# Optimization experiments

Hardware: AMD Instinct MI355X
Metric: run time of the kernel (lower is better)

Reference implementation:

```python
import jax, jax.numpy as jnp
import numpy as np

D_MODEL = 1024
N_HEADS = 16
D_K = D_MODEL // N_HEADS
THETA = 10000.0
MAX_SEQ = 2048


def _trunc_normal(key, shape, std):
    # approximate trunc_normal in [-3std, 3std] via clipping (init only; values irrelevant to math)
    return jnp.clip(jax.random.normal(key, shape) * std, -3 * std, 3 * std).astype(jnp.float32)


def setup_inputs() -> dict:
    key = jax.random.key(0)
    kx, kq, kk, kv, ko = jax.random.split(key, 5)
    std = np.sqrt(2.0 / (D_MODEL + D_MODEL))
    x = jax.random.normal(kx, (2, 2048, D_MODEL), dtype=jnp.float32)
    W_q = _trunc_normal(kq, (D_MODEL, D_MODEL), std)
    W_k = _trunc_normal(kk, (D_MODEL, D_MODEL), std)
    W_v = _trunc_normal(kv, (D_MODEL, D_MODEL), std)
    W_o = _trunc_normal(ko, (D_MODEL, D_MODEL), std)
    return {"x": x, "W_q": W_q, "W_k": W_k, "W_v": W_v, "W_o": W_o}


def _rope(x, positions):
    # x: [b, n, s, d_k]; interleaved even/odd pairing: (x0,x1),(x2,x3),...
    d = x.shape[-1]
    inv_freq = THETA ** (-2.0 * jnp.arange(0, d // 2, dtype=jnp.float32) / d)
    angles = positions.astype(jnp.float32)[:, None] * inv_freq[None, :]  # [s, d/2]
    cos, sin = jnp.cos(angles), jnp.sin(angles)
    xp = x.reshape(x.shape[:-1] + (d // 2, 2))
    x_even, x_odd = xp[..., 0], xp[..., 1]
    out_even = x_even * cos - x_odd * sin
    out_odd = x_even * sin + x_odd * cos
    return jnp.stack((out_even, out_odd), axis=-1).reshape(x.shape)


def reference(x, W_q, W_k, W_v, W_o):
    b, s, _ = x.shape
    def split_heads(t):
        return t.reshape(b, s, N_HEADS, D_K).transpose(0, 2, 1, 3)  # b n s d
    Q = split_heads(x @ W_q.T)
    K = split_heads(x @ W_k.T)
    V = split_heads(x @ W_v.T)
    pos = jnp.arange(s)
    Q = _rope(Q, pos)
    K = _rope(K, pos)
    score = jnp.einsum('bnqd,bnkd->bnqk', Q, K) / jnp.sqrt(jnp.float32(D_K))
    causal = jnp.triu(jnp.ones((s, s), dtype=bool), k=1)
    score = jnp.where(causal[None, None], -jnp.inf, score)
    attn = jax.nn.softmax(score, axis=-1)
    out = jnp.einsum('bnqk,bnkd->bnqd', attn, V)
    out = out.transpose(0, 2, 1, 3).reshape(b, s, D_MODEL)
    return out @ W_o.T
```

## Files before the change

### kernel.cpp

```cpp
#include <hip/hip_runtime.h>

typedef float f32x4 __attribute__((ext_vector_type(4)));
typedef __bf16 bf16x8 __attribute__((ext_vector_type(8)));

#define D_MODEL 1024
#define SEQ     2048
#define NB      2
#define NH      16
#define DK      64

__device__ __forceinline__ unsigned short f2bf(float f) {
    union { float f; unsigned int u; } un; un.f = f;
    unsigned int r = un.u + 0x7fffu + ((un.u >> 16) & 1u);
    return (unsigned short)(r >> 16);
}

__device__ __forceinline__ unsigned cvtpk(float lo, float hi) {
    unsigned r;
    asm("v_cvt_pk_bf16_f32 %0, %1, %2" : "=v"(r) : "v"(lo), "v"(hi));
    return r;
}

__device__ __forceinline__ void gload16(const void* g, void* l) {
    __builtin_amdgcn_global_load_lds((__attribute__((address_space(1))) void*)g,
                                     (__attribute__((address_space(3))) void*)l,
                                     16, 0, 0);
}

__global__ __launch_bounds__(256) void cast5(
    const float* __restrict__ x,  const float* __restrict__ wq,
    const float* __restrict__ wk, const float* __restrict__ wv,
    const float* __restrict__ wo,
    unsigned short* __restrict__ xb,  unsigned short* __restrict__ wqb,
    unsigned short* __restrict__ wkb, unsigned short* __restrict__ wvb,
    unsigned short* __restrict__ wob, float2* __restrict__ tab)
{
    if (blockIdx.y == 5) {
        int idx = blockIdx.x * 256 + threadIdx.x;
        if (idx < SEQ * 32) {
            int ss = idx >> 5, p = idx & 31;
            float freq = exp2f(-0.41524101186f * (float)p);
            float sn, cs;
            sincosf((float)ss * freq, &sn, &cs);
            tab[idx] = make_float2(cs, sn);
        }
        return;
    }
    const float* src; unsigned short* dst; int n8;
    switch (blockIdx.y) {
        case 0:  src = x;  dst = xb;  n8 = (NB*SEQ*D_MODEL)/8; break;
        case 1:  src = wq; dst = wqb; n8 = (D_MODEL*D_MODEL)/8; break;
        case 2:  src = wk; dst = wkb; n8 = (D_MODEL*D_MODEL)/8; break;
        case 3:  src = wv; dst = wvb; n8 = (D_MODEL*D_MODEL)/8; break;
        default: src = wo; dst = wob; n8 = (D_MODEL*D_MODEL)/8; break;
    }
    int stride = gridDim.x * blockDim.x;
    for (int i = blockIdx.x * blockDim.x + threadIdx.x; i < n8; i += stride) {
        const float4* p = (const float4*)src + (size_t)i * 2;
        float4 a = p[0], b = p[1];
        union { unsigned short h[8]; uint4 v; } u;
        u.h[0] = f2bf(a.x); u.h[1] = f2bf(a.y); u.h[2] = f2bf(a.z); u.h[3] = f2bf(a.w);
        u.h[4] = f2bf(b.x); u.h[5] = f2bf(b.y); u.h[6] = f2bf(b.z); u.h[7] = f2bf(b.w);
        ((uint4*)dst)[i] = u.v;
    }
}

template <int MODE, int BM, int BN>
__global__ __launch_bounds__(256) void gemm_bt(
    const unsigned short* __restrict__ A,
    const unsigned short* __restrict__ B0,
    const unsigned short* __restrict__ B1,
    const unsigned short* __restrict__ B2,
    float* __restrict__ outF,
    unsigned short* __restrict__ Qh,
    unsigned short* __restrict__ Kh,
    unsigned short* __restrict__ Vt,
    const float2* __restrict__ tab,
    int M, int K)
{
    constexpr int PER_STAGE = (BM + BN) / 64;
    constexpr int WM = BM / 2, WN = BN / 2;
    constexpr int FM = WM / 16, FN = WN / 16;
    __shared__ __align__(16) unsigned short SM[3 * (BM + BN) * 32];

    const int lane = threadIdx.x & 63;
    const int wid  = threadIdx.x >> 6;
    const int l15 = lane & 15, lhi = lane >> 4;

    const int L  = blockIdx.x;
    const int yl = L & 7;
    const int t  = L >> 3;
    const int bx = t & 7;
    const int t2 = t >> 3;
    int y, z;
    if constexpr (MODE == 1) { y = ((t2 & 3) << 3) | yl; z = t2 >> 2; }
    else                     { y = (t2 << 3) | yl;       z = 0;       }
    const int m0 = y * BM;
    const int n0 = bx * BN;
    const unsigned short* B = (z == 0) ? B0 : (z == 1) ? B1 : B2;
    const int waveM = (wid >> 1) * WM;
    const int waveN = (wid & 1) * WN;

    f32x4 acc[FM][FN];
    f32x4 zero = {0.f, 0.f, 0.f, 0.f};
#pragma unroll
    for (int m = 0; m < FM; ++m)
#pragma unroll
        for (int n = 0; n < FN; ++n) acc[m][n] = zero;

    const int lrow = lane >> 2;
    const int lcol = (lane & 3) * 8;

    auto STAGE = [&](int buf, int k0) {
        unsigned short* as = SM + buf * (BM + BN) * 32;
        unsigned short* bs = as + BM * 32;
#pragma unroll
        for (int q = 0; q < BM / 64; ++q) {
            int rbase = wid * (BM / 4) + q * 16;
            gload16(A + (size_t)(m0 + rbase + lrow) * K + k0 + lcol,
                    (char*)as + rbase * 64);
        }
#pragma unroll
        for (int q = 0; q < BN / 64; ++q) {
            int rbase = wid * (BN / 4) + q * 16;
            gload16(B + (size_t)(n0 + rbase + lrow) * K + k0 + lcol,
                    (char*)bs + rbase * 64);
        }
    };

    const int NK = K >> 5;
    STAGE(0, 0);
    STAGE(1, 32);

    for (int k = 0; k < NK; ++k) {
        if (k < NK - 1) {
            if constexpr (PER_STAGE == 4) asm volatile("s_waitcnt vmcnt(4)" ::: "memory");
            else                          asm volatile("s_waitcnt vmcnt(3)" ::: "memory");
        } else {
            asm volatile("s_waitcnt vmcnt(0)" ::: "memory");
        }
        __builtin_amdgcn_s_barrier();
        __builtin_amdgcn_sched_barrier(0);
        if (k + 2 < NK) STAGE((k + 2) % 3, (k + 2) << 5);

        const unsigned short* as = SM + (k % 3) * (BM + BN) * 32;
        const unsigned short* bs = as + BM * 32;
        bf16x8 af[FM], bfr[FN];
#pragma unroll
        for (int m = 0; m < FM; ++m)
            af[m] = *(const bf16x8*)(as + (waveM + m * 16 + l15) * 32 + lhi * 8);
#pragma unroll
        for (int n = 0; n < FN; ++n)
            bfr[n] = *(const bf16x8*)(bs + (waveN + n * 16 + l15) * 32 + lhi * 8);
        __builtin_amdgcn_s_setprio(1);
#pragma unroll
        for (int m = 0; m < FM; ++m)
#pragma unroll
            for (int n = 0; n < FN; ++n)
                acc[m][n] = __builtin_amdgcn_mfma_f32_16x16x32_bf16(af[m], bfr[n], acc[m][n], 0, 0, 0);
        __builtin_amdgcn_s_setprio(0);
    }

    if constexpr (MODE == 0) {
#pragma unroll
        for (int n = 0; n < FN; ++n) {
            int col = n0 + waveN + n * 16 + l15;
#pragma unroll
            for (int m = 0; m < FM; ++m) {
                int rowb = m0 + waveM + m * 16 + (lhi << 2);
#pragma unroll
                for (int r = 0; r < 4; ++r)
                    outF[(size_t)(rowb + r) * D_MODEL + col] = acc[m][n][r];
            }
        }
    } else {
        __syncthreads();
        unsigned short* Ct = ((unsigned short*)SM) + wid * 4608;
        const int colg0 = n0 + waveN;
        const int hh    = (colg0 >> 6) & (NH - 1);
        const int rowg0 = m0 + waveM;
        const int bb    = rowg0 >> 11;
        const size_t bhh = (size_t)(bb * NH + hh);

#pragma unroll
        for (int n = 0; n < 4; ++n) {
            int cl = n * 16 + l15;
#pragma unroll
            for (int m = 0; m < 4; ++m) {
#pragma unroll
                for (int r = 0; r < 4; ++r) {
                    float v  = acc[m][n][r];
                    float pv = __shfl_xor(v, 1);
                    int rl = m * 16 + (lhi << 2) + r;
                    if (z == 2) {
                        Ct[cl * 72 + rl] = f2bf(v);
                    } else {
                        int ss = (rowg0 + rl) & (SEQ - 1);
                        float2 cs = tab[(ss << 5) + (cl >> 1)];
                        float o = (cl & 1) ? (pv * cs.y + v * cs.x)
                                           : (v * cs.x - pv * cs.y);
                        if (z == 0) o *= 0.18033688011f;
                        Ct[rl * 72 + cl] = f2bf(o);
                    }
                }
            }
        }
        asm volatile("s_waitcnt lgkmcnt(0)" ::: "memory");

        const int lr = lane >> 3;
        const int lc = (lane & 7) << 3;
#pragma unroll
        for (int i = 0; i < 8; ++i) {
            int rl = i * 8 + lr;
            uint4 w = *(const uint4*)&Ct[rl * 72 + lc];
            if (z == 2) {
                int ss0 = rowg0 & (SEQ - 1);
                *(uint4*)(Vt + (bhh * DK + rl) * SEQ + ss0 + lc) = w;
            } else {
                int ss = (rowg0 + rl) & (SEQ - 1);
                unsigned short* dst = (z == 0) ? Qh : Kh;
                *(uint4*)(dst + (bhh * SEQ + ss) * DK + lc) = w;
            }
        }
    }
}

__global__ __launch_bounds__(256) void attn_kernel(
    const unsigned short* __restrict__ Qh,
    const unsigned short* __restrict__ Kh,
    const unsigned short* __restrict__ Vt,
    unsigned short* __restrict__ O)
{
    __shared__ unsigned short Ks[2][64 * 64];
    __shared__ unsigned short Vs[2][64 * 64];
    __shared__ unsigned short P[4][16 * 64];

    const int tid  = threadIdx.x;
    const int lane = tid & 63;
    const int wid  = tid >> 6;
    const int l15 = lane & 15, lhi = lane >> 4;

    const int Bk  = blockIdx.x;
    const int xcd = Bk & 7;
    const int r0  = Bk >> 3;
    const int bh  = (xcd << 2) | (r0 & 3);
    const int yq  = r0 >> 2;
    const int g   = yq >> 3, j = yq & 7;
    const int qt  = (g << 3) + ((g & 1) ? (7 - j) : j);
    const int b = bh >> 4, h = bh & 15;

    const unsigned short* Qb = Qh + (size_t)bh * SEQ * DK;
    const unsigned short* Kb = Kh + (size_t)bh * SEQ * DK;
    const unsigned short* Vb = Vt + (size_t)bh * DK * SEQ;

    auto STAGE = [&](int buf, int kv0s) {
#pragma unroll
        for (int c = 0; c < 2; ++c) {
            int ub = c * 256 + wid * 64;
            int u  = ub + lane;
            int kr = u >> 3;
            int kc = (u & 7) ^ (kr & 7);
            gload16(Kb + (size_t)(kv0s + kr) * DK + kc * 8, &Ks[buf][(size_t)ub * 8]);
        }
#pragma unroll
        for (int c = 0; c < 2; ++c) {
            int ub = c * 256 + wid * 64;
            int u  = ub + lane;
            int vr = u >> 3;
            int vc = (u & 7) ^ (vr & 7);
            gload16(Vb + (size_t)vr * SEQ + kv0s + vc * 8, &Vs[buf][(size_t)ub * 8]);
        }
    };

    const f32x4 zero = {0.f, 0.f, 0.f, 0.f};
    const f32x4 ninf = {-1e30f, -1e30f, -1e30f, -1e30f};

    STAGE(0, 0);
    int cur = 0;

    const int q0 = qt * 64;
    const int qw = q0 + wid * 16;

    bf16x8 qf[2];
#pragma unroll
    for (int kk = 0; kk < 2; ++kk)
        qf[kk] = *(const bf16x8*)(Qb + (size_t)(qw + l15) * DK + kk * 32 + lhi * 8);

    f32x4 oacc[4];
#pragma unroll
    for (int nd = 0; nd < 4; ++nd) oacc[nd] = zero;
    float mrow = -1e30f;
    float lrow = 0.f;

    for (int kt = 0; kt <= qt; ++kt) {
        const int kv0 = kt << 6;
        const bool diag = (kt == qt);
        const int nlim = diag ? (wid + 1) : 4;

        asm volatile("s_waitcnt vmcnt(0)" ::: "memory");
        __builtin_amdgcn_s_barrier();
        __builtin_amdgcn_sched_barrier(0);

        if (kt < qt) STAGE(cur ^ 1, kv0 + 64);

        f32x4 s[4];
#pragma unroll
        for (int n = 0; n < 4; ++n) s[n] = (n < nlim) ? zero : ninf;

        const int sw = l15 & 7;
        __builtin_amdgcn_s_setprio(1);
#pragma unroll
        for (int n = 0; n < 4; ++n) {
            if (n < nlim) {
                int rr = n * 16 + l15;
                bf16x8 k0 = *(const bf16x8*)&Ks[cur][rr * 64 + ((lhi ^ sw) << 3)];
                bf16x8 k1 = *(const bf16x8*)&Ks[cur][rr * 64 + (((4 + lhi) ^ sw) << 3)];
                s[n] = __builtin_amdgcn_mfma_f32_16x16x32_bf16(k0, qf[0], s[n], 0, 0, 0);
                s[n] = __builtin_amdgcn_mfma_f32_16x16x32_bf16(k1, qf[1], s[n], 0, 0, 0);
            }
        }
        __builtin_amdgcn_s_setprio(0);

        if (diag) {
            const int qg = qw + l15;
#pragma unroll
            for (int n = 0; n < 4; ++n) {
                if (n < nlim) {
#pragma unroll
                    for (int rr = 0; rr < 4; ++rr) {
                        int kg = kv0 + n * 16 + (lhi << 2) + rr;
                        if (kg > qg) s[n][rr] = -1e30f;
                    }
                }
            }
        }

        float mx = fmaxf(fmaxf(s[0][0], s[0][1]), fmaxf(s[0][2], s[0][3]));
#pragma unroll
        for (int n = 1; n < 4; ++n)
            mx = fmaxf(mx, fmaxf(fmaxf(s[n][0], s[n][1]), fmaxf(s[n][2], s[n][3])));
        mx = fmaxf(mx, __shfl_xor(mx, 16));
        mx = fmaxf(mx, __shfl_xor(mx, 32));

        float alpha = 1.f;
        const int allDefer = __all(mx <= mrow + 8.f);
        if (!allDefer) {
            float mn = fmaxf(mrow, mx);
            alpha = __builtin_amdgcn_exp2f(mrow - mn);
            mrow = mn;
        }

#pragma unroll
        for (int n = 0; n < 4; ++n)
#pragma unroll
            for (int rr = 0; rr < 4; ++rr)
                s[n][rr] = __builtin_amdgcn_exp2f(s[n][rr] - mrow);

        float rs = 0.f;
#pragma unroll
        for (int n = 0; n < 4; ++n)
            rs += (s[n][0] + s[n][1]) + (s[n][2] + s[n][3]);
        rs += __shfl_xor(rs, 16);
        rs += __shfl_xor(rs, 32);
        lrow = allDefer ? (lrow + rs) : (lrow * alpha + rs);

#pragma unroll
        for (int n = 0; n < 4; ++n) {
            uint2 pk;
            pk.x = cvtpk(s[n][0], s[n][1]);
            pk.y = cvtpk(s[n][2], s[n][3]);
            int cW = 2 * n + (lhi >> 1);
            *(uint2*)&P[wid][(l15 << 6) + ((cW ^ sw) << 3) + ((lhi & 1) << 2)] = pk;
        }

        if (!allDefer) {
            float a0 = __shfl(alpha, (lhi << 2) + 0);
            float a1 = __shfl(alpha, (lhi << 2) + 1);
            float a2 = __shfl(alpha, (lhi << 2) + 2);
            float a3 = __shfl(alpha, (lhi << 2) + 3);
#pragma unroll
            for (int nd = 0; nd < 4; ++nd) {
                oacc[nd][0] *= a0; oacc[nd][1] *= a1;
                oacc[nd][2] *= a2; oacc[nd][3] *= a3;
            }
        }

        asm volatile("s_waitcnt lgkmcnt(0)" ::: "memory");
        const int kklim = diag ? ((nlim + 1) >> 1) : 2;
        bf16x8 pa[2];
#pragma unroll
        for (int kk = 0; kk < 2; ++kk)
            if (kk < kklim)
                pa[kk] = *(const bf16x8*)&P[wid][(l15 << 6) + ((((kk << 2) + lhi) ^ sw) << 3)];

        __builtin_amdgcn_s_setprio(1);
#pragma unroll
        for (int nd = 0; nd < 4; ++nd)
#pragma unroll
            for (int kk = 0; kk < 2; ++kk)
                if (kk < kklim) {
                    int rd = nd * 16 + l15;
                    bf16x8 vf = *(const bf16x8*)&Vs[cur][rd * 64 + ((((kk << 2) + lhi) ^ sw) << 3)];
                    oacc[nd] = __builtin_amdgcn_mfma_f32_16x16x32_bf16(pa[kk], vf, oacc[nd], 0, 0, 0);
                }
        __builtin_amdgcn_s_setprio(0);

        cur ^= 1;
    }

    float inv = 1.f / lrow;
    float i0 = __shfl(inv, (lhi << 2) + 0);
    float i1 = __shfl(inv, (lhi << 2) + 1);
    float i2 = __shfl(inv, (lhi << 2) + 2);
    float i3 = __shfl(inv, (lhi << 2) + 3);
#pragma unroll
    for (int nd = 0; nd < 4; ++nd) {
        int d = nd * 16 + l15;
        int rowb = qw + (lhi << 2);
        O[((size_t)(b * SEQ + rowb + 0)) * D_MODEL + h * DK + d] = f2bf(oacc[nd][0] * i0);
        O[((size_t)(b * SEQ + rowb + 1)) * D_MODEL + h * DK + d] = f2bf(oacc[nd][1] * i1);
        O[((size_t)(b * SEQ + rowb + 2)) * D_MODEL + h * DK + d] = f2bf(oacc[nd][2] * i2);
        O[((size_t)(b * SEQ + rowb + 3)) * D_MODEL + h * DK + d] = f2bf(oacc[nd][3] * i3);
    }
}

extern "C" void kernel_launch(void* const* d_in, const int* in_sizes, int n_in,
                              void* d_out, int out_size, void* d_ws, size_t ws_size,
                              hipStream_t stream)
{
    const float* x  = (const float*)d_in[0];
    const float* Wq = (const float*)d_in[1];
    const float* Wk = (const float*)d_in[2];
    const float* Wv = (const float*)d_in[3];
    const float* Wo = (const float*)d_in[4];
    float* out = (float*)d_out;

    char* ws = (char*)d_ws;
    unsigned short* xb  = (unsigned short*)(ws);
    unsigned short* Wqb = (unsigned short*)(ws + ( 8ull << 20));
    unsigned short* Wkb = (unsigned short*)(ws + (10ull << 20));
    unsigned short* Wvb = (unsigned short*)(ws + (12ull << 20));
    unsigned short* Wob = (unsigned short*)(ws + (14ull << 20));
    unsigned short* Qh  = (unsigned short*)(ws + (16ull << 20));
    unsigned short* Kh  = (unsigned short*)(ws + (24ull << 20));
    unsigned short* Vt  = (unsigned short*)(ws + (32ull << 20));
    float2*         tab = (float2*)(ws + (40ull << 20));
    unsigned short* attn = xb;

    cast5<<<dim3(512, 6), 256, 0, stream>>>(x, Wq, Wk, Wv, Wo, xb, Wqb, Wkb, Wvb, Wob, tab);

    gemm_bt<1, 128, 128><<<768, 256, 0, stream>>>(
        xb, Wqb, Wkb, Wvb, nullptr, Qh, Kh, Vt, tab, NB * SEQ, D_MODEL);

    attn_kernel<<<1024, 256, 0, stream>>>(Qh, Kh, Vt, attn);

    gemm_bt<0, 64, 128><<<512, 256, 0, stream>>>(
        attn, Wob, Wob, Wob, out, nullptr, nullptr, nullptr, nullptr, NB * SEQ, D_MODEL);
}
```

Before: 116.7 us.

## Pair causal q-tiles per block and triple-buffer K/V tiles

Each attention block now handles two query tiles, pi and 31-pi, so every block does the same 33 KV-tile iterations. This balances the causal triangle's work and halves the grid to 512 blocks. The K/V staging moves from double to triple buffering with a lookahead of two tiles and a partial vmcnt wait, which hides more load latency. The cost is more shared memory per block (lower possible occupancy) and fewer blocks to fill the GPU.

Result: no change. 115.9 us (-0.7%).

```diff
diff --git a/kernel.cpp b/kernel.cpp
--- a/kernel.cpp
+++ b/kernel.cpp
@@ -231,8 +231,8 @@
     const unsigned short* __restrict__ Vt,
     unsigned short* __restrict__ O)
 {
-    __shared__ unsigned short Ks[2][64 * 64];
-    __shared__ unsigned short Vs[2][64 * 64];
+    __shared__ unsigned short Ks[3][64 * 64];
+    __shared__ unsigned short Vs[3][64 * 64];
     __shared__ unsigned short P[4][16 * 64];
 
     const int tid  = threadIdx.x;
@@ -240,18 +240,21 @@
     const int wid  = tid >> 6;
     const int l15 = lane & 15, lhi = lane >> 4;
 
-    const int Bk  = blockIdx.x;
-    const int xcd = Bk & 7;
-    const int r0  = Bk >> 3;
+    const int L   = blockIdx.x;
+    const int xcd = L & 7;
+    const int r0  = L >> 3;
     const int bh  = (xcd << 2) | (r0 & 3);
-    const int yq  = r0 >> 2;
-    const int g   = yq >> 3, j = yq & 7;
-    const int qt  = (g << 3) + ((g & 1) ? (7 - j) : j);
+    const int pi  = r0 >> 2;
     const int b = bh >> 4, h = bh & 15;
 
     const unsigned short* Qb = Qh + (size_t)bh * SEQ * DK;
     const unsigned short* Kb = Kh + (size_t)bh * SEQ * DK;
     const unsigned short* Vb = Vt + (size_t)bh * DK * SEQ;
+
+    const int NT0 = pi + 1;
+    const int NTT = 33;
+
+    auto kv_of = [&](int g) { return (g < NT0 ? g : g - NT0) << 6; };
 
     auto STAGE = [&](int buf, int kv0s) {
 #pragma unroll
@@ -261,166 +264,165 @@
             int kr = u >> 3;
             int kc = (u & 7) ^ (kr & 7);
             gload16(Kb + (size_t)(kv0s + kr) * DK + kc * 8, &Ks[buf][(size_t)ub * 8]);
-        }
-#pragma unroll
-        for (int c = 0; c < 2; ++c) {
-            int ub = c * 256 + wid * 64;
-            int u  = ub + lane;
-            int vr = u >> 3;
-            int vc = (u & 7) ^ (vr & 7);
-            gload16(Vb + (size_t)vr * SEQ + kv0s + vc * 8, &Vs[buf][(size_t)ub * 8]);
+            gload16(Vb + (size_t)kr * SEQ + kv0s + kc * 8, &Vs[buf][(size_t)ub * 8]);
         }
     };
 
     const f32x4 zero = {0.f, 0.f, 0.f, 0.f};
     const f32x4 ninf = {-1e30f, -1e30f, -1e30f, -1e30f};
+    const int sw = l15 & 7;
 
     STAGE(0, 0);
-    int cur = 0;
-
-    const int q0 = qt * 64;
-    const int qw = q0 + wid * 16;
-
-    bf16x8 qf[2];
-#pragma unroll
-    for (int kk = 0; kk < 2; ++kk)
-        qf[kk] = *(const bf16x8*)(Qb + (size_t)(qw + l15) * DK + kk * 32 + lhi * 8);
-
-    f32x4 oacc[4];
-#pragma unroll
-    for (int nd = 0; nd < 4; ++nd) oacc[nd] = zero;
-    float mrow = -1e30f;
-    float lrow = 0.f;
-
-    for (int kt = 0; kt <= qt; ++kt) {
-        const int kv0 = kt << 6;
-        const bool diag = (kt == qt);
-        const int nlim = diag ? (wid + 1) : 4;
-
-        asm volatile("s_waitcnt vmcnt(0)" ::: "memory");
-        __builtin_amdgcn_s_barrier();
-        __builtin_amdgcn_sched_barrier(0);
-
-        if (kt < qt) STAGE(cur ^ 1, kv0 + 64);
-
-        f32x4 s[4];
-#pragma unroll
-        for (int n = 0; n < 4; ++n) s[n] = (n < nlim) ? zero : ninf;
-
-        const int sw = l15 & 7;
-        __builtin_amdgcn_s_setprio(1);
-#pragma unroll
-        for (int n = 0; n < 4; ++n) {
-            if (n < nlim) {
-                int rr = n * 16 + l15;
-                bf16x8 k0 = *(const bf16x8*)&Ks[cur][rr * 64 + ((lhi ^ sw) << 3)];
-                bf16x8 k1 = *(const bf16x8*)&Ks[cur][rr * 64 + (((4 + lhi) ^ sw) << 3)];
-                s[n] = __builtin_amdgcn_mfma_f32_16x16x32_bf16(k0, qf[0], s[n], 0, 0, 0);
-                s[n] = __builtin_amdgcn_mfma_f32_16x16x32_bf16(k1, qf[1], s[n], 0, 0, 0);
-            }
-        }
-        __builtin_amdgcn_s_setprio(0);
-
-        if (diag) {
-            const int qg = qw + l15;
+    STAGE(1, kv_of(1));
+    int g = 0;
+
+    for (int ph = 0; ph < 2; ++ph) {
+        const int qt = ph ? (31 - pi) : pi;
+        const int q0 = qt << 6;
+        const int qw = q0 + wid * 16;
+        const int lastkt = qt;
+
+        bf16x8 qf[2];
+#pragma unroll
+        for (int kk = 0; kk < 2; ++kk)
+            qf[kk] = *(const bf16x8*)(Qb + (size_t)(qw + l15) * DK + kk * 32 + lhi * 8);
+
+        f32x4 oacc[4];
+#pragma unroll
+        for (int nd = 0; nd < 4; ++nd) oacc[nd] = zero;
+        float mrow = -1e30f;
+        float lrow = 0.f;
+
+        for (int kt = 0; kt <= lastkt; ++kt, ++g) {
+            const int kv0 = kt << 6;
+            const bool diag = (kt == lastkt);
+            const int nlim = diag ? (wid + 1) : 4;
+
+            if (g < NTT - 1) asm volatile("s_waitcnt vmcnt(4)" ::: "memory");
+            else             asm volatile("s_waitcnt vmcnt(0)" ::: "memory");
+            __builtin_amdgcn_s_barrier();
+            __builtin_amdgcn_sched_barrier(0);
+            if (g + 2 < NTT) STAGE((g + 2) % 3, kv_of(g + 2));
+
+            const unsigned short* Kc = Ks[g % 3];
+            const unsigned short* Vc = Vs[g % 3];
+
+            f32x4 s[4];
+#pragma unroll
+            for (int n = 0; n < 4; ++n) s[n] = (n < nlim) ? zero : ninf;
+
+            __builtin_amdgcn_s_setprio(1);
 #pragma unroll
             for (int n = 0; n < 4; ++n) {
                 if (n < nlim) {
-#pragma unroll
-                    for (int rr = 0; rr < 4; ++rr) {
-                        int kg = kv0 + n * 16 + (lhi << 2) + rr;
-                        if (kg > qg) s[n][rr] = -1e30f;
+                    int rr = n * 16 + l15;
+                    bf16x8 k0 = *(const bf16x8*)&Kc[rr * 64 + ((lhi ^ sw) << 3)];
+                    bf16x8 k1 = *(const bf16x8*)&Kc[rr * 64 + (((4 + lhi) ^ sw) << 3)];
+                    s[n] = __builtin_amdgcn_mfma_f32_16x16x32_bf16(k0, qf[0], s[n], 0, 0, 0);
+                    s[n] = __builtin_amdgcn_mfma_f32_16x16x32_bf16(k1, qf[1], s[n], 0, 0, 0);
+                }
+            }
+            __builtin_amdgcn_s_setprio(0);
+
+            if (diag) {
+                const int qg = qw + l15;
+#pragma unroll
+                for (int n = 0; n < 4; ++n) {
+                    if (n < nlim) {
+#pragma unroll
+                        for (int rr = 0; rr < 4; ++rr) {
+                            int kg = kv0 + n * 16 + (lhi << 2) + rr;
+                            if (kg > qg) s[n][rr] = -1e30f;
+                        }
                     }
                 }
             }
-        }
-
-        float mx = fmaxf(fmaxf(s[0][0], s[0][1]), fmaxf(s[0][2], s[0][3]));
-#pragma unroll
-        for (int n = 1; n < 4; ++n)
-            mx = fmaxf(mx, fmaxf(fmaxf(s[n][0], s[n][1]), fmaxf(s[n][2], s[n][3])));
-        mx = fmaxf(mx, __shfl_xor(mx, 16));
-        mx = fmaxf(mx, __shfl_xor(mx, 32));
-
-        float alpha = 1.f;
-        const int allDefer = __all(mx <= mrow + 8.f);
-        if (!allDefer) {
-            float mn = fmaxf(mrow, mx);
-            alpha = __builtin_amdgcn_exp2f(mrow - mn);
-            mrow = mn;
-        }
-
-#pragma unroll
-        for (int n = 0; n < 4; ++n)
-#pragma unroll
-            for (int rr = 0; rr < 4; ++rr)
-                s[n][rr] = __builtin_amdgcn_exp2f(s[n][rr] - mrow);
-
-        float rs = 0.f;
-#pragma unroll
-        for (int n = 0; n < 4; ++n)
-            rs += (s[n][0] + s[n][1]) + (s[n][2] + s[n][3]);
-        rs += __shfl_xor(rs, 16);
-        rs += __shfl_xor(rs, 32);
-        lrow = allDefer ? (lrow + rs) : (lrow * alpha + rs);
-
-#pragma unroll
-        for (int n = 0; n < 4; ++n) {
-            uint2 pk;
-            pk.x = cvtpk(s[n][0], s[n][1]);
-            pk.y = cvtpk(s[n][2], s[n][3]);
-            int cW = 2 * n + (lhi >> 1);
-            *(uint2*)&P[wid][(l15 << 6) + ((cW ^ sw) << 3) + ((lhi & 1) << 2)] = pk;
-        }
-
-        if (!allDefer) {
-            float a0 = __shfl(alpha, (lhi << 2) + 0);
-            float a1 = __shfl(alpha, (lhi << 2) + 1);
-            float a2 = __shfl(alpha, (lhi << 2) + 2);
-            float a3 = __shfl(alpha, (lhi << 2) + 3);
-#pragma unroll
-            for (int nd = 0; nd < 4; ++nd) {
-                oacc[nd][0] *= a0; oacc[nd][1] *= a1;
-                oacc[nd][2] *= a2; oacc[nd][3] *= a3;
-            }
-        }
-
-        asm volatile("s_waitcnt lgkmcnt(0)" ::: "memory");
-        const int kklim = diag ? ((nlim + 1) >> 1) : 2;
-        bf16x8 pa[2];
-#pragma unroll
-        for (int kk = 0; kk < 2; ++kk)
-            if (kk < kklim)
-                pa[kk] = *(const bf16x8*)&P[wid][(l15 << 6) + ((((kk << 2) + lhi) ^ sw) << 3)];
-
-        __builtin_amdgcn_s_setprio(1);
-#pragma unroll
-        for (int nd = 0; nd < 4; ++nd)
+
+            float mx = fmaxf(fmaxf(s[0][0], s[0][1]), fmaxf(s[0][2], s[0][3]));
+#pragma unroll
+            for (int n = 1; n < 4; ++n)
+                mx = fmaxf(mx, fmaxf(fmaxf(s[n][0], s[n][1]), fmaxf(s[n][2], s[n][3])));
+            mx = fmaxf(mx, __shfl_xor(mx, 16));
+            mx = fmaxf(mx, __shfl_xor(mx, 32));
+
+            float alpha = 1.f;
+            const int allDefer = __all(mx <= mrow + 8.f);
+            if (!allDefer) {
+                float mn = fmaxf(mrow, mx);
+                alpha = __builtin_amdgcn_exp2f(mrow - mn);
+                mrow = mn;
+            }
+
+#pragma unroll
+            for (int n = 0; n < 4; ++n)
+#pragma unroll
+                for (int rr = 0; rr < 4; ++rr)
+                    s[n][rr] = __builtin_amdgcn_exp2f(s[n][rr] - mrow);
+
+            float rs = 0.f;
+#pragma unroll
+            for (int n = 0; n < 4; ++n)
+                rs += (s[n][0] + s[n][1]) + (s[n][2] + s[n][3]);
+            rs += __shfl_xor(rs, 16);
+            rs += __shfl_xor(rs, 32);
+            lrow = allDefer ? (lrow + rs) : (lrow * alpha + rs);
+
+#pragma unroll
+            for (int n = 0; n < 4; ++n) {
+                uint2 pk;
+                pk.x = cvtpk(s[n][0], s[n][1]);
+                pk.y = cvtpk(s[n][2], s[n][3]);
+                int cW = 2 * n + (lhi >> 1);
+                *(uint2*)&P[wid][(l15 << 6) + ((cW ^ sw) << 3) + ((lhi & 1) << 2)] = pk;
+            }
+
+            if (!allDefer) {
+                float a0 = __shfl(alpha, (lhi << 2) + 0);
+                float a1 = __shfl(alpha, (lhi << 2) + 1);
+                float a2 = __shfl(alpha, (lhi << 2) + 2);
+                float a3 = __shfl(alpha, (lhi << 2) + 3);
+#pragma unroll
+                for (int nd = 0; nd < 4; ++nd) {
+                    oacc[nd][0] *= a0; oacc[nd][1] *= a1;
+                    oacc[nd][2] *= a2; oacc[nd][3] *= a3;
+                }
+            }
+
+            asm volatile("s_waitcnt lgkmcnt(0)" ::: "memory");
+            const int kklim = diag ? ((nlim + 1) >> 1) : 2;
+            bf16x8 pa[2];
 #pragma unroll
             for (int kk = 0; kk < 2; ++kk)
-                if (kk < kklim) {
-                    int rd = nd * 16 + l15;
-                    bf16x8 vf = *(const bf16x8*)&Vs[cur][rd * 64 + ((((kk << 2) + lhi) ^ sw) << 3)];
-                    oacc[nd] = __builtin_amdgcn_mfma_f32_16x16x32_bf16(pa[kk], vf, oacc[nd], 0, 0, 0);
-                }
-        __builtin_amdgcn_s_setprio(0);
-
-        cur ^= 1;
-    }
-
-    float inv = 1.f / lrow;
-    float i0 = __shfl(inv, (lhi << 2) + 0);
-    float i1 = __shfl(inv, (lhi << 2) + 1);
-    float i2 = __shfl(inv, (lhi << 2) + 2);
-    float i3 = __shfl(inv, (lhi << 2) + 3);
-#pragma unroll
-    for (int nd = 0; nd < 4; ++nd) {
-        int d = nd * 16 + l15;
-        int rowb = qw + (lhi << 2);
-        O[((size_t)(b * SEQ + rowb + 0)) * D_MODEL + h * DK + d] = f2bf(oacc[nd][0] * i0);
-        O[((size_t)(b * SEQ + rowb + 1)) * D_MODEL + h * DK + d] = f2bf(oacc[nd][1] * i1);
-        O[((size_t)(b * SEQ + rowb + 2)) * D_MODEL + h * DK + d] = f2bf(oacc[nd][2] * i2);
-        O[((size_t)(b * SEQ + rowb + 3)) * D_MODEL + h * DK + d] = f2bf(oacc[nd][3] * i3);
+                if (kk < kklim)
+                    pa[kk] = *(const bf16x8*)&P[wid][(l15 << 6) + ((((kk << 2) + lhi) ^ sw) << 3)];
+
+            __builtin_amdgcn_s_setprio(1);
+#pragma unroll
+            for (int nd = 0; nd < 4; ++nd)
+#pragma unroll
+                for (int kk = 0; kk < 2; ++kk)
+                    if (kk < kklim) {
+                        int rd = nd * 16 + l15;
+                        bf16x8 vf = *(const bf16x8*)&Vc[rd * 64 + ((((kk << 2) + lhi) ^ sw) << 3)];
+                        oacc[nd] = __builtin_amdgcn_mfma_f32_16x16x32_bf16(pa[kk], vf, oacc[nd], 0, 0, 0);
+                    }
+            __builtin_amdgcn_s_setprio(0);
+        }
+
+        float inv = 1.f / lrow;
+        float i0 = __shfl(inv, (lhi << 2) + 0);
+        float i1 = __shfl(inv, (lhi << 2) + 1);
+        float i2 = __shfl(inv, (lhi << 2) + 2);
+        float i3 = __shfl(inv, (lhi << 2) + 3);
+#pragma unroll
+        for (int nd = 0; nd < 4; ++nd) {
+            int d = nd * 16 + l15;
+            int rowb = qw + (lhi << 2);
+            O[((size_t)(b * SEQ + rowb + 0)) * D_MODEL + h * DK + d] = f2bf(oacc[nd][0] * i0);
+            O[((size_t)(b * SEQ + rowb + 1)) * D_MODEL + h * DK + d] = f2bf(oacc[nd][1] * i1);
+            O[((size_t)(b * SEQ + rowb + 2)) * D_MODEL + h * DK + d] = f2bf(oacc[nd][2] * i2);
+            O[((size_t)(b * SEQ + rowb + 3)) * D_MODEL + h * DK + d] = f2bf(oacc[nd][3] * i3);
+        }
     }
 }
 
@@ -452,7 +454,7 @@
     gemm_bt<1, 128, 128><<<768, 256, 0, stream>>>(
         xb, Wqb, Wkb, Wvb, nullptr, Qh, Kh, Vt, tab, NB * SEQ, D_MODEL);
 
-    attn_kernel<<<1024, 256, 0, stream>>>(Qh, Kh, Vt, attn);
+    attn_kernel<<<512, 256, 0, stream>>>(Qh, Kh, Vt, attn);
 
     gemm_bt<0, 64, 128><<<512, 256, 0, stream>>>(
         attn, Wob, Wob, Wob, out, nullptr, nullptr, nullptr, nullptr, NB * SEQ, D_MODEL);
```
